# Optimization experiments

Measured on AMD Instinct MI355X. Metric: run time of the kernel, lower is better.

Reference implementation:

```python
import jax, jax.numpy as jnp
import numpy as np

N = 50000        # nodes
E = 1_600_000    # edges
IN = 64          # in_feats
H = 128          # h_feats
L = 5            # num_layers
G = 512          # graphs in batch
C = 10           # num_classes


def setup_inputs() -> dict:
    key = jax.random.key(0)
    ks = jax.random.split(key, 12)
    s = 0.05
    x = jax.random.normal(ks[0], (N, IN), jnp.float32)
    edge_index = jax.random.randint(ks[1], (2, E), 0, N, dtype=jnp.int32)
    batch = jnp.sort(jax.random.randint(ks[2], (N,), 0, G, dtype=jnp.int32))
    edge_weight = jax.random.uniform(ks[3], (E,), jnp.float32)
    # GatedGraphConv params: per-layer mixing weight + shared GRUCell
    weight = jax.random.normal(ks[4], (L, H, H), jnp.float32) * s
    w_ih = jax.random.normal(ks[5], (3 * H, H), jnp.float32) * s
    w_hh = jax.random.normal(ks[6], (3 * H, H), jnp.float32) * s
    b_ih = jax.random.normal(ks[7], (3 * H,), jnp.float32) * s
    b_hh = jax.random.normal(ks[8], (3 * H,), jnp.float32) * s
    # MLP head
    dense1_w = jax.random.normal(ks[9], (4 * H, H), jnp.float32) * s
    dense1_b = jnp.zeros((4 * H,), jnp.float32)
    dense2_w = jax.random.normal(ks[10], (C, 4 * H), jnp.float32) * s
    dense2_b = jnp.zeros((C,), jnp.float32)
    return dict(x=x, edge_index=edge_index, batch=batch, edge_weight=edge_weight,
                weight=weight, w_ih=w_ih, w_hh=w_hh, b_ih=b_ih, b_hh=b_hh,
                dense1_w=dense1_w, dense1_b=dense1_b,
                dense2_w=dense2_w, dense2_b=dense2_b)


def _gru_cell(m, h, w_ih, w_hh, b_ih, b_hh):
    # torch.nn.GRUCell(input=m, hidden=h)
    gi = m @ w_ih.T + b_ih
    gh = h @ w_hh.T + b_hh
    i_r, i_z, i_n = jnp.split(gi, 3, axis=-1)
    h_r, h_z, h_n = jnp.split(gh, 3, axis=-1)
    r = jax.nn.sigmoid(i_r + h_r)
    z = jax.nn.sigmoid(i_z + h_z)
    n = jnp.tanh(i_n + r * h_n)
    return (1.0 - z) * n + z * h


def reference(x, edge_index, batch, edge_weight, weight, w_ih, w_hh, b_ih, b_hh,
              dense1_w, dense1_b, dense2_w, dense2_b):
    src, dst = edge_index[0], edge_index[1]
    # pad in_feats -> h_feats (PyG GatedGraphConv)
    h = jnp.pad(x, ((0, 0), (0, H - IN)))
    for l in range(L):
        m = h @ weight[l]                          # [N, H]
        msg = m[src] * edge_weight[:, None]        # gather + edge gating [E, H]
        agg = jax.ops.segment_sum(msg, dst, num_segments=N)  # scatter-add
        h = _gru_cell(agg, h, w_ih, w_hh, b_ih, b_hh)
    pooled = jax.ops.segment_max(h, batch, num_segments=G)   # global max pool [G, H]
    # dropout is identity in eval mode
    hid = jax.nn.relu(pooled @ dense1_w.T + dense1_b)
    out = hid @ dense2_w.T + dense2_b
    return out
```

## Files before the change

kernel.cpp:

```cpp
#include <hip/hip_runtime.h>
#include <hip/hip_bf16.h>

#define NN 50000
#define NE 1600000
#define FIN 64
#define H 128
#define NL 5
#define NG 512
#define NC 10

typedef __attribute__((ext_vector_type(8))) short short8;
typedef __attribute__((ext_vector_type(4))) float f32x4;

#define OFF_H2A   0
#define OFF_H2B   3200000
#define OFF_CUR   6400000
#define OFF_OFF   6450176
#define OFF_CSR   6500352
#define OFF_POOL  8900352
#define OFF_FWF   8965888
#define OFF_FWHH  9088768

__device__ __forceinline__ short rne_bf16(float f){
    unsigned u = __float_as_uint(f);
    unsigned r = (u + 0x7FFFu + ((u >> 16) & 1u)) >> 16;
    return (short)r;
}
__device__ __forceinline__ float bf_lo(unsigned v){ return __uint_as_float(v << 16); }
__device__ __forceinline__ float bf_hi(unsigned v){ return __uint_as_float(v & 0xFFFF0000u); }


__global__ void k_hist(const int* __restrict__ ei, int* __restrict__ cnt){
    int e = blockIdx.x*256 + threadIdx.x;
    if (e < NE) atomicAdd(&cnt[ei[NE + e]], 1);
}

__global__ void k_scan(int* __restrict__ cur, int* __restrict__ off){
    __shared__ int s[1024];
    int t = threadIdx.x;
    const int CH = 49;
    int base = t*CH;
    int m = (NN + 1) - base; if (m > CH) m = CH; if (m < 0) m = 0;
    int sum = 0;
    for (int i = 0; i < m; ++i) sum += (cur[base + i] + 15) & ~15;
    s[t] = sum; __syncthreads();
    for (int o = 1; o < 1024; o <<= 1){
        int v = (t >= o) ? s[t - o] : 0; __syncthreads();
        s[t] += v; __syncthreads();
    }
    int run = s[t] - sum;
    for (int i = 0; i < m; ++i){
        int c = (cur[base + i] + 15) & ~15;
        off[base + i] = run;
        cur[base + i] = run;
        run += c;
    }
}

__global__ void k_fill(const int* __restrict__ ei, const float* __restrict__ ew,
                       int* __restrict__ cur, unsigned* __restrict__ csr){
    int e = blockIdx.x*256 + threadIdx.x;
    if (e >= NE) return;
    int src = ei[e], dst = ei[NE + e];
    int pos = atomicAdd(&cur[dst], 1);
    csr[pos] = (unsigned)src | (((unsigned)(ushort)rne_bf16(ew[e])) << 16);
}


__global__ void k_pad(const float* __restrict__ x, ushort* __restrict__ h2a){
    int idx = blockIdx.x*256 + threadIdx.x;
    int n = idx >> 7, f = idx & 127;
    float v = (f < FIN) ? x[n*FIN + f] : 0.f;
    h2a[idx] = (ushort)rne_bf16(v);
}

__global__ void k_fuse(const float* __restrict__ W, const float* __restrict__ wih,
                       short* __restrict__ fwf){
    int idx = blockIdx.x*256 + threadIdx.x;
    int l = idx / 49152;
    int r = idx % 49152;
    int k = r / 384, n = r % 384;
    const float* wl = W + l*16384 + k*128;
    const float* wi = wih + n*128;
    float acc = 0.f;
    for (int c = 0; c < 128; ++c) acc += wl[c]*wi[c];
    int lane = ((k>>3)&3)*16 + (n&15);
    fwf[l*49152 + (((n>>4)*4 + (k>>5))*64 + lane)*8 + (k&7)] = rne_bf16(acc);
}

__global__ void k_cvt_whh(const float* __restrict__ whh, short* __restrict__ fwhh){
    int idx = blockIdx.x*256 + threadIdx.x;
    int k = idx / 384, n = idx % 384;
    float v = whh[n*128 + k];
    int lane = ((k>>3)&3)*16 + (n&15);
    fwhh[(((n>>4)*4 + (k>>5))*64 + lane)*8 + (k&7)] = rne_bf16(v);
}

__global__ void k_init_pool(unsigned* __restrict__ p){
    p[blockIdx.x*256 + threadIdx.x] = 0x007FFFFFu;
}

__global__ __launch_bounds__(256)
void k_layer(const ushort* __restrict__ h2r, ushort* __restrict__ h2w,
             const int* __restrict__ off, const unsigned* __restrict__ csr,
             const short* __restrict__ fwf, const short* __restrict__ fwhh,
             const float* __restrict__ b_ih, const float* __restrict__ b_hh,
             const int* __restrict__ batch, unsigned* __restrict__ pooled,
             int last){
    __shared__ ushort tl[16*136];
    int tid = threadIdx.x;
    int n0 = blockIdx.x * 16;
    int wave = tid >> 6, lane = tid & 63;
    int lane_lo = lane & 15, quad = lane >> 4;
    int grp = lane >> 4, fl = lane & 15;

    for (int sub = 0; sub < 4; ++sub){
        int node = n0 + wave*4 + sub;
        int start = __builtin_amdgcn_readfirstlane(off[node]);
        int end   = __builtin_amdgcn_readfirstlane(off[node + 1]);
        float a0=0.f,a1=0.f,a2=0.f,a3=0.f,a4=0.f,a5=0.f,a6=0.f,a7=0.f;
        const ushort* hb = h2r + fl*8;
        for (int i = start; i < end; i += 16){
            uint4 c = *(const uint4*)(csr + i + grp*4);
            uint4 v0 = *(const uint4*)(hb + (c.x & 0xFFFFu)*H);
            uint4 v1 = *(const uint4*)(hb + (c.y & 0xFFFFu)*H);
            uint4 v2 = *(const uint4*)(hb + (c.z & 0xFFFFu)*H);
            uint4 v3 = *(const uint4*)(hb + (c.w & 0xFFFFu)*H);
            float w0 = bf_hi(c.x), w1 = bf_hi(c.y), w2 = bf_hi(c.z), w3 = bf_hi(c.w);
            a0 += w0*bf_lo(v0.x); a1 += w0*bf_hi(v0.x); a2 += w0*bf_lo(v0.y); a3 += w0*bf_hi(v0.y);
            a4 += w0*bf_lo(v0.z); a5 += w0*bf_hi(v0.z); a6 += w0*bf_lo(v0.w); a7 += w0*bf_hi(v0.w);
            a0 += w1*bf_lo(v1.x); a1 += w1*bf_hi(v1.x); a2 += w1*bf_lo(v1.y); a3 += w1*bf_hi(v1.y);
            a4 += w1*bf_lo(v1.z); a5 += w1*bf_hi(v1.z); a6 += w1*bf_lo(v1.w); a7 += w1*bf_hi(v1.w);
            a0 += w2*bf_lo(v2.x); a1 += w2*bf_hi(v2.x); a2 += w2*bf_lo(v2.y); a3 += w2*bf_hi(v2.y);
            a4 += w2*bf_lo(v2.z); a5 += w2*bf_hi(v2.z); a6 += w2*bf_lo(v2.w); a7 += w2*bf_hi(v2.w);
            a0 += w3*bf_lo(v3.x); a1 += w3*bf_hi(v3.x); a2 += w3*bf_lo(v3.y); a3 += w3*bf_hi(v3.y);
            a4 += w3*bf_lo(v3.z); a5 += w3*bf_hi(v3.z); a6 += w3*bf_lo(v3.w); a7 += w3*bf_hi(v3.w);
        }
        a0 += __shfl_xor(a0,16); a1 += __shfl_xor(a1,16); a2 += __shfl_xor(a2,16); a3 += __shfl_xor(a3,16);
        a4 += __shfl_xor(a4,16); a5 += __shfl_xor(a5,16); a6 += __shfl_xor(a6,16); a7 += __shfl_xor(a7,16);
        a0 += __shfl_xor(a0,32); a1 += __shfl_xor(a1,32); a2 += __shfl_xor(a2,32); a3 += __shfl_xor(a3,32);
        a4 += __shfl_xor(a4,32); a5 += __shfl_xor(a5,32); a6 += __shfl_xor(a6,32); a7 += __shfl_xor(a7,32);
        if (lane < 16){
            short8 hbv;
            hbv[0]=rne_bf16(a0); hbv[1]=rne_bf16(a1); hbv[2]=rne_bf16(a2); hbv[3]=rne_bf16(a3);
            hbv[4]=rne_bf16(a4); hbv[5]=rne_bf16(a5); hbv[6]=rne_bf16(a6); hbv[7]=rne_bf16(a7);
            *(short8*)(tl + (wave*4 + sub)*136 + fl*8) = hbv;
        }
    }
    __syncthreads();

    f32x4 ai[6], ah[6];
    #pragma unroll
    for (int i = 0; i < 6; ++i){ ai[i] = (f32x4){0.f,0.f,0.f,0.f}; ah[i] = (f32x4){0.f,0.f,0.f,0.f}; }

    const ushort* arow_t = tl + lane_lo*136;
    const ushort* arow_h = h2r + (size_t)(n0 + lane_lo)*H;
    #pragma unroll
    for (int kt = 0; kt < 4; ++kt){
        short8 at  = *(const short8*)(arow_t + kt*32 + quad*8);
        short8 ahh = *(const short8*)(arow_h + kt*32 + quad*8);
        #pragma unroll
        for (int s = 0; s < 3; ++s){
            #pragma unroll
            for (int t16 = 0; t16 < 2; ++t16){
                int tile = (s*8 + wave*2 + t16)*4 + kt;
                short8 bi = *(const short8*)(fwf  + tile*512 + lane*8);
                short8 bh = *(const short8*)(fwhh + tile*512 + lane*8);
                ai[s*2+t16] = __builtin_amdgcn_mfma_f32_16x16x32_bf16(at,  bi, ai[s*2+t16], 0, 0, 0);
                ah[s*2+t16] = __builtin_amdgcn_mfma_f32_16x16x32_bf16(ahh, bh, ah[s*2+t16], 0, 0, 0);
            }
        }
    }

    #pragma unroll
    for (int t16 = 0; t16 < 2; ++t16){
        int j = wave*32 + t16*16 + lane_lo;
        float bir = b_ih[j], biz = b_ih[128 + j], bin_ = b_ih[256 + j];
        float bhr = b_hh[j], bhz = b_hh[128 + j], bhn  = b_hh[256 + j];
        #pragma unroll
        for (int r = 0; r < 4; ++r){
            int row = n0 + quad*4 + r;
            float gir = ai[t16][r]     + bir, ghr = ah[t16][r]     + bhr;
            float giz = ai[2 + t16][r] + biz, ghz = ah[2 + t16][r] + bhz;
            float gin = ai[4 + t16][r] + bin_, ghn = ah[4 + t16][r] + bhn;
            float rr = 1.f/(1.f + __expf(-(gir + ghr)));
            float zz = 1.f/(1.f + __expf(-(giz + ghz)));
            float nn = tanhf(gin + rr*ghn);
            float ho = __uint_as_float(((unsigned)h2r[(size_t)row*H + j]) << 16);
            float hv = (1.f - zz)*nn + zz*ho;
            if (!last){
                h2w[(size_t)row*H + j] = (ushort)rne_bf16(hv);
            } else {
                int g = batch[row];
                unsigned u = __float_as_uint(hv);
                u = (u & 0x80000000u) ? ~u : (u | 0x80000000u);
                atomicMax(pooled + g*H + j, u);
            }
        }
    }
}


__global__ void k_head(const unsigned* __restrict__ pooled,
                       const float* __restrict__ d1w, const float* __restrict__ d1b,
                       const float* __restrict__ d2w, const float* __restrict__ d2b,
                       float* __restrict__ out){
    __shared__ float sp[128];
    __shared__ float shid[512];
    int g = blockIdx.x, tid = threadIdx.x;
    if (tid < 128){
        unsigned u = pooled[g*H + tid];
        sp[tid] = __uint_as_float((u & 0x80000000u) ? (u ^ 0x80000000u) : ~u);
    }
    __syncthreads();
    for (int o = tid; o < 512; o += 256){
        float acc = d1b[o];
        for (int k = 0; k < H; ++k) acc += sp[k] * d1w[o*H + k];
        shid[o] = fmaxf(acc, 0.f);
    }
    __syncthreads();
    if (tid < NC){
        float acc = d2b[tid];
        for (int o = 0; o < 512; ++o) acc += shid[o] * d2w[tid*512 + o];
        out[g*NC + tid] = acc;
    }
}

extern "C" void kernel_launch(void* const* d_in, const int* in_sizes, int n_in,
                              void* d_out, int out_size, void* d_ws, size_t ws_size,
                              hipStream_t stream){
    const float* x     = (const float*)d_in[0];
    const int*   ei    = (const int*)d_in[1];
    const int*   batch = (const int*)d_in[2];
    const float* ew    = (const float*)d_in[3];
    const float* W     = (const float*)d_in[4];
    const float* wih   = (const float*)d_in[5];
    const float* whh   = (const float*)d_in[6];
    const float* bih   = (const float*)d_in[7];
    const float* bhh   = (const float*)d_in[8];
    const float* d1w   = (const float*)d_in[9];
    const float* d1b   = (const float*)d_in[10];
    const float* d2w   = (const float*)d_in[11];
    const float* d2b   = (const float*)d_in[12];
    float* out = (float*)d_out;

    float*  ws  = (float*)d_ws;
    ushort* h2a = (ushort*)(ws + OFF_H2A);
    ushort* h2b = (ushort*)(ws + OFF_H2B);
    int*    cur = (int*)(ws + OFF_CUR);
    int*    off = (int*)(ws + OFF_OFF);
    unsigned* csr = (unsigned*)(ws + OFF_CSR);
    unsigned* pooled = (unsigned*)(ws + OFF_POOL);
    short*  fwf  = (short*)(ws + OFF_FWF);
    short*  fwhh = (short*)(ws + OFF_FWHH);

    hipMemsetAsync(cur, 0, 50176*sizeof(int), stream);
    hipMemsetAsync(csr, 0, 2400000*sizeof(unsigned), stream);
    k_hist<<<6250, 256, 0, stream>>>(ei, cur);
    k_scan<<<1, 1024, 0, stream>>>(cur, off);
    k_fill<<<6250, 256, 0, stream>>>(ei, ew, cur, csr);

    k_fuse<<<960, 256, 0, stream>>>(W, wih, fwf);
    k_cvt_whh<<<192, 256, 0, stream>>>(whh, fwhh);
    k_pad<<<25000, 256, 0, stream>>>(x, h2a);
    k_init_pool<<<256, 256, 0, stream>>>(pooled);

    for (int l = 0; l < NL; ++l){
        ushort* h2r = (l & 1) ? h2b : h2a;
        ushort* h2w = (l & 1) ? h2a : h2b;
        k_layer<<<3125, 256, 0, stream>>>(h2r, h2w, off, csr,
                                          fwf + (size_t)l*49152, fwhh, bih, bhh,
                                          batch, pooled, (l == NL-1) ? 1 : 0);
    }

    k_head<<<NG, 256, 0, stream>>>(pooled, d1w, d1b, d2w, d2b, out);
}
```

Baseline: 938.0 us.

## Use 8 waves per layer block, vectorize pad and weight-fuse kernels

k_layer now runs 512 threads per 16-node block. Each wave gathers 2 nodes instead of 4 and computes one 16-column output tile per gate instead of two, which halves per-wave serial work and accumulator registers. k_pad writes 8 bf16 values per thread from float4 loads, and k_fuse uses float4 dot products, to cut preprocessing instruction count. The larger block size may change occupancy and raises the cost of the block-wide barrier.

```diff
diff --git a/kernel.cpp b/kernel.cpp
--- a/kernel.cpp
+++ b/kernel.cpp
@@ -69,9 +69,17 @@
 
 __global__ void k_pad(const float* __restrict__ x, ushort* __restrict__ h2a){
     int idx = blockIdx.x*256 + threadIdx.x;
-    int n = idx >> 7, f = idx & 127;
-    float v = (f < FIN) ? x[n*FIN + f] : 0.f;
-    h2a[idx] = (ushort)rne_bf16(v);
+    int n = idx >> 4, f8 = idx & 15;
+    short8 v;
+    if (f8 < 8){
+        float4 a = *(const float4*)(x + n*FIN + f8*8);
+        float4 b = *(const float4*)(x + n*FIN + f8*8 + 4);
+        v[0]=rne_bf16(a.x); v[1]=rne_bf16(a.y); v[2]=rne_bf16(a.z); v[3]=rne_bf16(a.w);
+        v[4]=rne_bf16(b.x); v[5]=rne_bf16(b.y); v[6]=rne_bf16(b.z); v[7]=rne_bf16(b.w);
+    } else {
+        v[0]=0; v[1]=0; v[2]=0; v[3]=0; v[4]=0; v[5]=0; v[6]=0; v[7]=0;
+    }
+    *(short8*)(h2a + idx*8) = v;
 }
 
 __global__ void k_fuse(const float* __restrict__ W, const float* __restrict__ wih,
@@ -80,10 +88,14 @@
     int l = idx / 49152;
     int r = idx % 49152;
     int k = r / 384, n = r % 384;
-    const float* wl = W + l*16384 + k*128;
-    const float* wi = wih + n*128;
+    const float4* wl = (const float4*)(W + l*16384 + k*128);
+    const float4* wi = (const float4*)(wih + n*128);
     float acc = 0.f;
-    for (int c = 0; c < 128; ++c) acc += wl[c]*wi[c];
+    #pragma unroll 8
+    for (int c = 0; c < 32; ++c){
+        float4 a = wl[c], b = wi[c];
+        acc += a.x*b.x + a.y*b.y + a.z*b.z + a.w*b.w;
+    }
     int lane = ((k>>3)&3)*16 + (n&15);
     fwf[l*49152 + (((n>>4)*4 + (k>>5))*64 + lane)*8 + (k&7)] = rne_bf16(acc);
 }
@@ -100,7 +112,7 @@
     p[blockIdx.x*256 + threadIdx.x] = 0x007FFFFFu;
 }
 
-__global__ __launch_bounds__(256)
+__global__ __launch_bounds__(512)
 void k_layer(const ushort* __restrict__ h2r, ushort* __restrict__ h2w,
              const int* __restrict__ off, const unsigned* __restrict__ csr,
              const short* __restrict__ fwf, const short* __restrict__ fwhh,
@@ -114,8 +126,8 @@
     int lane_lo = lane & 15, quad = lane >> 4;
     int grp = lane >> 4, fl = lane & 15;
 
-    for (int sub = 0; sub < 4; ++sub){
-        int node = n0 + wave*4 + sub;
+    for (int sub = 0; sub < 2; ++sub){
+        int node = n0 + wave*2 + sub;
         int start = __builtin_amdgcn_readfirstlane(off[node]);
         int end   = __builtin_amdgcn_readfirstlane(off[node + 1]);
         float a0=0.f,a1=0.f,a2=0.f,a3=0.f,a4=0.f,a5=0.f,a6=0.f,a7=0.f;
@@ -144,14 +156,14 @@
             short8 hbv;
             hbv[0]=rne_bf16(a0); hbv[1]=rne_bf16(a1); hbv[2]=rne_bf16(a2); hbv[3]=rne_bf16(a3);
             hbv[4]=rne_bf16(a4); hbv[5]=rne_bf16(a5); hbv[6]=rne_bf16(a6); hbv[7]=rne_bf16(a7);
-            *(short8*)(tl + (wave*4 + sub)*136 + fl*8) = hbv;
+            *(short8*)(tl + (wave*2 + sub)*136 + fl*8) = hbv;
         }
     }
     __syncthreads();
 
-    f32x4 ai[6], ah[6];
+    f32x4 ai[3], ah[3];
     #pragma unroll
-    for (int i = 0; i < 6; ++i){ ai[i] = (f32x4){0.f,0.f,0.f,0.f}; ah[i] = (f32x4){0.f,0.f,0.f,0.f}; }
+    for (int i = 0; i < 3; ++i){ ai[i] = (f32x4){0.f,0.f,0.f,0.f}; ah[i] = (f32x4){0.f,0.f,0.f,0.f}; }
 
     const ushort* arow_t = tl + lane_lo*136;
     const ushort* arow_h = h2r + (size_t)(n0 + lane_lo)*H;
@@ -161,28 +173,24 @@
         short8 ahh = *(const short8*)(arow_h + kt*32 + quad*8);
         #pragma unroll
         for (int s = 0; s < 3; ++s){
-            #pragma unroll
-            for (int t16 = 0; t16 < 2; ++t16){
-                int tile = (s*8 + wave*2 + t16)*4 + kt;
-                short8 bi = *(const short8*)(fwf  + tile*512 + lane*8);
-                short8 bh = *(const short8*)(fwhh + tile*512 + lane*8);
-                ai[s*2+t16] = __builtin_amdgcn_mfma_f32_16x16x32_bf16(at,  bi, ai[s*2+t16], 0, 0, 0);
-                ah[s*2+t16] = __builtin_amdgcn_mfma_f32_16x16x32_bf16(ahh, bh, ah[s*2+t16], 0, 0, 0);
-            }
-        }
-    }
-
-    #pragma unroll
-    for (int t16 = 0; t16 < 2; ++t16){
-        int j = wave*32 + t16*16 + lane_lo;
+            int tile = (s*8 + wave)*4 + kt;
+            short8 bi = *(const short8*)(fwf  + tile*512 + lane*8);
+            short8 bh = *(const short8*)(fwhh + tile*512 + lane*8);
+            ai[s] = __builtin_amdgcn_mfma_f32_16x16x32_bf16(at,  bi, ai[s], 0, 0, 0);
+            ah[s] = __builtin_amdgcn_mfma_f32_16x16x32_bf16(ahh, bh, ah[s], 0, 0, 0);
+        }
+    }
+
+    {
+        int j = wave*16 + lane_lo;
         float bir = b_ih[j], biz = b_ih[128 + j], bin_ = b_ih[256 + j];
         float bhr = b_hh[j], bhz = b_hh[128 + j], bhn  = b_hh[256 + j];
         #pragma unroll
         for (int r = 0; r < 4; ++r){
             int row = n0 + quad*4 + r;
-            float gir = ai[t16][r]     + bir, ghr = ah[t16][r]     + bhr;
-            float giz = ai[2 + t16][r] + biz, ghz = ah[2 + t16][r] + bhz;
-            float gin = ai[4 + t16][r] + bin_, ghn = ah[4 + t16][r] + bhn;
+            float gir = ai[0][r] + bir, ghr = ah[0][r] + bhr;
+            float giz = ai[1][r] + biz, ghz = ah[1][r] + bhz;
+            float gin = ai[2][r] + bin_, ghn = ah[2][r] + bhn;
             float rr = 1.f/(1.f + __expf(-(gir + ghr)));
             float zz = 1.f/(1.f + __expf(-(giz + ghz)));
             float nn = tanhf(gin + rr*ghn);
@@ -262,13 +270,13 @@
 
     k_fuse<<<960, 256, 0, stream>>>(W, wih, fwf);
     k_cvt_whh<<<192, 256, 0, stream>>>(whh, fwhh);
-    k_pad<<<25000, 256, 0, stream>>>(x, h2a);
+    k_pad<<<3125, 256, 0, stream>>>(x, h2a);
     k_init_pool<<<256, 256, 0, stream>>>(pooled);
 
     for (int l = 0; l < NL; ++l){
         ushort* h2r = (l & 1) ? h2b : h2a;
         ushort* h2w = (l & 1) ? h2a : h2b;
-        k_layer<<<3125, 256, 0, stream>>>(h2r, h2w, off, csr,
+        k_layer<<<3125, 512, 0, stream>>>(h2r, h2w, off, csr,
                                           fwf + (size_t)l*49152, fwhh, bih, bhh,
                                           batch, pooled, (l == NL-1) ? 1 : 0);
     }
```

Measured after the change: 864.5 us. 1.09x faster.
